# Performance work log

Measured on AMD Instinct MI355X. Metric: run time of the kernel, lower is better.

Reference implementation:

```python
import jax, jax.numpy as jnp
import numpy as np

INIT_RANGE = 0.02

def setup_inputs() -> dict:
    key = jax.random.key(0)
    ks = jax.random.split(key, 5)
    B, S, D, H, Dh = 4, 2048, 768, 12, 64
    residual = jax.random.normal(ks[0], (B, S, D), dtype=jnp.float32)
    W_Q = jax.random.normal(ks[1], (H, D, Dh), dtype=jnp.float32) * INIT_RANGE
    W_K = jax.random.normal(ks[2], (H, D, Dh), dtype=jnp.float32) * INIT_RANGE
    W_V = jax.random.normal(ks[3], (H, D, Dh), dtype=jnp.float32) * INIT_RANGE
    W_O = jax.random.normal(ks[4], (H, Dh, D), dtype=jnp.float32) * INIT_RANGE
    b_Q = jnp.zeros((H, Dh), dtype=jnp.float32)
    b_K = jnp.zeros((H, Dh), dtype=jnp.float32)
    b_V = jnp.zeros((H, Dh), dtype=jnp.float32)
    b_O = jnp.zeros((D,), dtype=jnp.float32)
    return {"residual": residual, "W_Q": W_Q, "W_K": W_K, "W_V": W_V,
            "W_O": W_O, "b_Q": b_Q, "b_K": b_K, "b_V": b_V, "b_O": b_O}

def reference(residual, W_Q, W_K, W_V, W_O, b_Q, b_K, b_V, b_O):
    # residual: [b, s, d]; W_{Q,K,V}: [h, d, dh]; W_O: [h, dh, d]
    d_head = W_Q.shape[-1]
    q = jnp.einsum('bsd,hde->bshe', residual, W_Q) + b_Q  # [b, s, h, dh]
    k = jnp.einsum('bsd,hde->bshe', residual, W_K) + b_K
    v = jnp.einsum('bsd,hde->bshe', residual, W_V) + b_V
    scores = jnp.einsum('bqhe,bkhe->bhqk', q, k) / jnp.sqrt(jnp.float32(d_head))
    S = residual.shape[1]
    causal = jnp.tril(jnp.ones((S, S), dtype=bool))  # True where attending allowed
    scores = jnp.where(causal, scores, -jnp.inf)
    pattern = jax.nn.softmax(scores, axis=-1)  # [b, h, q, k]
    z = jnp.einsum('bkhe,bhqk->bqhe', v, pattern)  # [b, q, h, dh]
    attn_out = jnp.einsum('bqhe,hed->bqd', z, W_O) + b_O
    return attn_out
```

## Files before the change

kernel.cpp:

```cpp
#include <hip/hip_runtime.h>

typedef short short8 __attribute__((ext_vector_type(8)));
typedef float floatx4 __attribute__((ext_vector_type(4)));
typedef unsigned short ushort_t;


__device__ inline ushort_t f2bf(float f) {
  union { float f; unsigned u; } x; x.f = f;
  unsigned u = x.u;
  unsigned r = u + 0x7fffu + ((u >> 16) & 1u);
  return (ushort_t)(r >> 16);
}

__device__ inline unsigned pk2(float a, float b) {
  union { float f; unsigned u; } x, y; x.f = a; y.f = b;
  return ((x.u + 0x8000u) >> 16) | ((y.u + 0x8000u) & 0xffff0000u);
}

__device__ inline float fexp2(float x) {
#if __has_builtin(__builtin_amdgcn_exp2f)
  return __builtin_amdgcn_exp2f(x);
#else
  return exp2f(x);
#endif
}

__device__ inline void async16(const void* g, void* l) {
  __builtin_amdgcn_global_load_lds((const __attribute__((address_space(1))) void*)g,
                                   (__attribute__((address_space(3))) void*)l,
                                   16, 0, 0);
}


__global__ __launch_bounds__(256) void conv_prep(
    const float* __restrict__ x, ushort_t* __restrict__ rx,
    const float* __restrict__ wq, const float* __restrict__ wk, const float* __restrict__ wv,
    const float* __restrict__ wo,
    const float* __restrict__ bq, const float* __restrict__ bk, const float* __restrict__ bv,
    ushort_t* __restrict__ wqkvT, ushort_t* __restrict__ woT, float* __restrict__ bqkv)
{
  __shared__ ushort_t t[64 * 72];
  const int tid = threadIdx.x;
  const int bid0 = blockIdx.x;
  if (bid0 < 6144) {
    int i = bid0 * 256 + tid;
    float4 f = ((const float4*)x)[i];
    ushort4 o;
    o.x = f2bf(f.x); o.y = f2bf(f.y); o.z = f2bf(f.z); o.w = f2bf(f.w);
    ((ushort4*)rx)[i] = o;
    return;
  }
  const int bid = bid0 - 6144;
  if (bid < 432) {
    int m = bid / 144, rem = bid % 144;
    int h = rem / 12, dt = rem % 12;
    int d0 = dt * 64;
    const float* w = (m == 0) ? wq : ((m == 1) ? wk : wv);
    const float* src = w + ((size_t)h * 768 + d0) * 64;
#pragma unroll
    for (int i = 0; i < 4; ++i) {
      int task = i * 256 + tid;
      int row = task >> 4, c4 = task & 15;
      float4 f = *(const float4*)(src + row * 64 + c4 * 4);
      ushort4 o4;
      o4.x = f2bf(f.x); o4.y = f2bf(f.y); o4.z = f2bf(f.z); o4.w = f2bf(f.w);
      *(ushort4*)&t[row * 72 + c4 * 4] = o4;
    }
    __syncthreads();
    ushort_t* dst = wqkvT + ((size_t)m * 768 + h * 64) * 768 + d0;
#pragma unroll
    for (int i = 0; i < 2; ++i) {
      int task = i * 256 + tid;
      int e = task >> 3, sc = task & 7;
      short8 d8;
#pragma unroll
      for (int j = 0; j < 8; ++j) d8[j] = (short)t[(sc * 8 + j) * 72 + e];
      *(short8*)(dst + (size_t)e * 768 + sc * 8) = d8;
    }
  } else if (bid < 576) {
    int b2 = bid - 432;
    int het = b2 / 12, dt = b2 % 12;
    int he0 = het * 64, d0 = dt * 64;
    const float* src = wo + (size_t)he0 * 768 + d0;
#pragma unroll
    for (int i = 0; i < 4; ++i) {
      int task = i * 256 + tid;
      int row = task >> 4, c4 = task & 15;
      float4 f = *(const float4*)(src + (size_t)row * 768 + c4 * 4);
      ushort4 o4;
      o4.x = f2bf(f.x); o4.y = f2bf(f.y); o4.z = f2bf(f.z); o4.w = f2bf(f.w);
      *(ushort4*)&t[row * 72 + c4 * 4] = o4;
    }
    __syncthreads();
    ushort_t* dst = woT + (size_t)d0 * 768 + he0;
#pragma unroll
    for (int i = 0; i < 2; ++i) {
      int task = i * 256 + tid;
      int dd = task >> 3, sc = task & 7;
      short8 d8;
#pragma unroll
      for (int j = 0; j < 8; ++j) d8[j] = (short)t[(sc * 8 + j) * 72 + dd];
      *(short8*)(dst + (size_t)dd * 768 + sc * 8) = d8;
    }
  } else {
    for (int idx = tid; idx < 2304; idx += 256) {
      int m = idx / 768, rem = idx - m * 768;
      const float* bp = (m == 0) ? bq : ((m == 1) ? bk : bv);
      bqkv[idx] = bp[rem];
    }
  }
}


__global__ __launch_bounds__(256) void gemm_qkv(
    const ushort_t* __restrict__ A, const ushort_t* __restrict__ Bt,
    const float* __restrict__ bias,
    ushort_t* __restrict__ q, ushort_t* __restrict__ k, ushort_t* __restrict__ vt)
{
  __shared__ ushort_t sh[17408];
  const int tid = threadIdx.x;
  const int wave = tid >> 6, lane = tid & 63;
  const int ln15 = lane & 15, quad = lane >> 4;
  const int id = blockIdx.x;
  const int xk = id & 7, j = id >> 3;
  const int bx = (xk >> 1) * 16 + (j & 15);
  const int by = (xk & 1) * 9 + (j >> 4);
  const int row0 = bx * 128, col0 = by * 128;
  const int wm = (wave >> 1) * 64, wn = (wave & 1) * 64;
  const int c0 = wave * 2;

  const ushort_t* gA0 = A + (size_t)(row0 + c0 * 16 + (lane >> 2)) * 768 + (lane & 3) * 8;
  const ushort_t* gB0 = Bt + (size_t)(col0 + c0 * 16 + (lane >> 2)) * 768 + (lane & 3) * 8;

  floatx4 acc[4][4];
#pragma unroll
  for (int mi = 0; mi < 4; ++mi)
#pragma unroll
    for (int ni = 0; ni < 4; ++ni)
      acc[mi][ni] = (floatx4){0.f, 0.f, 0.f, 0.f};

  async16(gA0, &sh[c0 * 512]);
  async16(gA0 + 16 * 768, &sh[c0 * 512 + 512]);
  async16(gB0, &sh[8192 + c0 * 512]);
  async16(gB0 + 16 * 768, &sh[8192 + c0 * 512 + 512]);
  __syncthreads();

  for (int kt = 0; kt < 24; ++kt) {
    const int buf = kt & 1;
    if (kt + 1 < 24) {
      ushort_t* dA = &sh[(buf ^ 1) * 4096];
      ushort_t* dB = &sh[8192 + (buf ^ 1) * 4096];
      async16(gA0 + (kt + 1) * 32, dA + c0 * 512);
      async16(gA0 + (kt + 1) * 32 + 16 * 768, dA + c0 * 512 + 512);
      async16(gB0 + (kt + 1) * 32, dB + c0 * 512);
      async16(gB0 + (kt + 1) * 32 + 16 * 768, dB + c0 * 512 + 512);
    }
    const ushort_t* sA = &sh[buf * 4096];
    const ushort_t* sB = &sh[8192 + buf * 4096];
    short8 af[4], bfv[4];
#pragma unroll
    for (int mi = 0; mi < 4; ++mi)
      af[mi] = *(const short8*)&sA[(wm + mi * 16 + ln15) * 32 + quad * 8];
#pragma unroll
    for (int ni = 0; ni < 4; ++ni)
      bfv[ni] = *(const short8*)&sB[(wn + ni * 16 + ln15) * 32 + quad * 8];
#pragma unroll
    for (int mi = 0; mi < 4; ++mi)
#pragma unroll
      for (int ni = 0; ni < 4; ++ni)
        acc[mi][ni] = __builtin_amdgcn_mfma_f32_16x16x32_bf16(af[mi], bfv[ni], acc[mi][ni], 0, 0, 0);
    __syncthreads();
  }

  if (col0 < 1536) {
    const float qscale = 0.125f * 1.44269504f;
#pragma unroll
    for (int mi = 0; mi < 4; ++mi) {
#pragma unroll
      for (int ni = 0; ni < 4; ++ni) {
        int gr = row0 + wm + mi * 16 + quad * 4;
        int gc = col0 + wn + ni * 16 + ln15;
        float bia = bias[gc];
        int m = gc >> 9 >> 1;
        m = gc / 768;
        int rem = gc - m * 768;
        int h = rem >> 6, e = rem & 63;
        ushort_t* dp = (m == 0) ? q : k;
#pragma unroll
        for (int r = 0; r < 4; ++r) {
          float val = acc[mi][ni][r] + bia;
          int rr = gr + r;
          int bb = rr >> 11, ss = rr & 2047;
          size_t dst = ((size_t)((bb * 12 + h) * 2048 + ss) << 6) + e;
          dp[dst] = f2bf((m == 0) ? val * qscale : val);
        }
      }
    }
  } else {
#pragma unroll
    for (int mi = 0; mi < 4; ++mi) {
#pragma unroll
      for (int ni = 0; ni < 4; ++ni) {
        int col = wn + ni * 16 + ln15;
        int rowb = wm + mi * 16 + quad * 4;
        float bia = bias[col0 + col];
        ushort4 w4;
        w4.x = f2bf(acc[mi][ni][0] + bia);
        w4.y = f2bf(acc[mi][ni][1] + bia);
        w4.z = f2bf(acc[mi][ni][2] + bia);
        w4.w = f2bf(acc[mi][ni][3] + bia);
        *(ushort4*)&sh[col * 136 + rowb] = w4;
      }
    }
    __syncthreads();
    const int relc0 = col0 - 1536;
    const int bb = row0 >> 11, s0 = row0 & 2047;
#pragma unroll
    for (int i = 0; i < 8; ++i) {
      int g = i * 256 + tid;
      int col = g >> 4, chunk = g & 15;
      short8 d = *(const short8*)&sh[col * 136 + chunk * 8];
      int hh = (relc0 + col) >> 6;
      int ee = col & 63;
      *(short8*)(vt + (((size_t)(bb * 12 + hh) * 64 + ee) << 11) + s0 + chunk * 8) = d;
    }
  }
}


__global__ __launch_bounds__(256) void gemm_out(
    const ushort_t* __restrict__ A, const ushort_t* __restrict__ Bt,
    const float* __restrict__ bias, float* __restrict__ outf)
{
  __shared__ ushort_t lA[2][64 * 32];
  __shared__ ushort_t lB[2][128 * 32];
  const int tid = threadIdx.x;
  const int wave = tid >> 6, lane = tid & 63;
  const int ln15 = lane & 15, quad = lane >> 4;
  const int id = blockIdx.x;
  const int xk = id & 7, j = id >> 3;
  const int bx = xk * 16 + (j & 15);
  const int by = j >> 4;
  const int row0 = bx * 64, col0 = by * 128;
  const int wm = (wave >> 1) * 32, wn = (wave & 1) * 64;
  const int cb = wave * 2;

  const ushort_t* gA0 = A + (size_t)(row0 + wave * 16 + (lane >> 2)) * 768 + (lane & 3) * 8;
  const ushort_t* gB0 = Bt + (size_t)(col0 + cb * 16 + (lane >> 2)) * 768 + (lane & 3) * 8;

  floatx4 acc[2][4];
#pragma unroll
  for (int mi = 0; mi < 2; ++mi)
#pragma unroll
    for (int ni = 0; ni < 4; ++ni)
      acc[mi][ni] = (floatx4){0.f, 0.f, 0.f, 0.f};

  async16(gA0, &lA[0][wave * 512]);
  async16(gB0, &lB[0][cb * 512]);
  async16(gB0 + 16 * 768, &lB[0][cb * 512 + 512]);
  __syncthreads();

  for (int kt = 0; kt < 24; ++kt) {
    const int buf = kt & 1;
    if (kt + 1 < 24) {
      async16(gA0 + (kt + 1) * 32, &lA[buf ^ 1][wave * 512]);
      async16(gB0 + (kt + 1) * 32, &lB[buf ^ 1][cb * 512]);
      async16(gB0 + (kt + 1) * 32 + 16 * 768, &lB[buf ^ 1][cb * 512 + 512]);
    }
    short8 af[2], bfv[4];
#pragma unroll
    for (int mi = 0; mi < 2; ++mi)
      af[mi] = *(const short8*)&lA[buf][(wm + mi * 16 + ln15) * 32 + quad * 8];
#pragma unroll
    for (int ni = 0; ni < 4; ++ni)
      bfv[ni] = *(const short8*)&lB[buf][(wn + ni * 16 + ln15) * 32 + quad * 8];
#pragma unroll
    for (int mi = 0; mi < 2; ++mi)
#pragma unroll
      for (int ni = 0; ni < 4; ++ni)
        acc[mi][ni] = __builtin_amdgcn_mfma_f32_16x16x32_bf16(af[mi], bfv[ni], acc[mi][ni], 0, 0, 0);
    __syncthreads();
  }

#pragma unroll
  for (int mi = 0; mi < 2; ++mi) {
#pragma unroll
    for (int ni = 0; ni < 4; ++ni) {
      int gr = row0 + wm + mi * 16 + quad * 4;
      int gc = col0 + wn + ni * 16 + ln15;
      float bia = bias[gc];
#pragma unroll
      for (int r = 0; r < 4; ++r)
        outf[(size_t)(gr + r) * 768 + gc] = acc[mi][ni][r] + bia;
    }
  }
}


__device__ inline short8 frag_ld(const ushort_t* t, int row, int ch) {
  return *(const short8*)&t[row * 64 + (((ch ^ row) & 7) * 8)];
}

__global__ __launch_bounds__(256) void attn3(
    const ushort_t* __restrict__ Q, const ushort_t* __restrict__ K,
    const ushort_t* __restrict__ VT, ushort_t* __restrict__ Z)
{
  __shared__ ushort_t lK[2][64 * 64];
  __shared__ ushort_t lV[2][64 * 64];
  __shared__ ushort_t lPQ[128 * 64];
  const int tid = threadIdx.x;
  const int wave = tid >> 6, lane = tid & 63;
  const int ln15 = lane & 15, quad = lane >> 4;
  const int bi = blockIdx.x;
  const int bh = bi % 48;
  const int t = 15 - (bi / 48);
  const int h = bh % 12, b = bh / 12;
  const size_t base = (size_t)bh * 2048 * 64;
  const ushort_t* Qp = Q + base + (size_t)t * 128 * 64;
  const ushort_t* Kp = K + base;
  const ushort_t* Vp = VT + base;
  const int nk = 2 * t + 2;

  const int srow = tid >> 3, slch = tid & 7;
  const int sc_ = slch ^ (srow & 7);

#pragma unroll
  for (int i = 0; i < 4; ++i) {
    int task = i * 256 + tid;
    int row = task >> 3;
    int c = slch ^ (row & 7);
    async16(Qp + row * 64 + c * 8, &lPQ[task * 8]);
  }
  async16(Kp + (size_t)srow * 64 + sc_ * 8, &lK[0][tid * 8]);
  async16(Kp + (size_t)(srow + 32) * 64 + sc_ * 8, &lK[0][(256 + tid) * 8]);
  async16(Vp + (size_t)srow * 2048 + sc_ * 8, &lV[0][tid * 8]);
  async16(Vp + (size_t)(srow + 32) * 2048 + sc_ * 8, &lV[0][(256 + tid) * 8]);

  const ushort_t* kPre0 = Kp + (size_t)(64 + srow) * 64 + sc_ * 8;
  const ushort_t* kPre1 = kPre0 + 32 * 64;
  const ushort_t* vPre0 = Vp + (size_t)srow * 2048 + 64 + sc_ * 8;
  const ushort_t* vPre1 = vPre0 + 32 * 2048;

  __syncthreads();
  short8 qf[2][2];
#pragma unroll
  for (int c = 0; c < 2; ++c) {
    qf[c][0] = frag_ld(lPQ, wave * 32 + c * 16 + ln15, quad);
    qf[c][1] = frag_ld(lPQ, wave * 32 + c * 16 + ln15, quad + 4);
  }
  __syncthreads();

  float l_i[2] = {0.f, 0.f};
  floatx4 o[2][4];
#pragma unroll
  for (int c = 0; c < 2; ++c)
#pragma unroll
    for (int et = 0; et < 4; ++et) o[c][et] = (floatx4){0.f, 0.f, 0.f, 0.f};

  ushort_t* lPw = lPQ + wave * 2048;
  const int qg0 = t * 128 + wave * 32 + ln15;

  for (int kt = 0; kt < nk; ++kt) {
    const int buf = kt & 1;
    if (kt + 1 < nk) {
      ushort_t* dK = lK[buf ^ 1];
      ushort_t* dV = lV[buf ^ 1];
      async16(kPre0, dK + tid * 8);
      async16(kPre1, dK + (256 + tid) * 8);
      async16(vPre0, dV + tid * 8);
      async16(vPre1, dV + (256 + tid) * 8);
      kPre0 += 4096; kPre1 += 4096; vPre0 += 64; vPre1 += 64;
    }

    floatx4 st[2][4];
#pragma unroll
    for (int ni = 0; ni < 4; ++ni) {
      short8 kf0 = frag_ld(lK[buf], ni * 16 + ln15, quad);
      short8 kf1 = frag_ld(lK[buf], ni * 16 + ln15, quad + 4);
#pragma unroll
      for (int c = 0; c < 2; ++c) {
        floatx4 z4 = (floatx4){0.f, 0.f, 0.f, 0.f};
        z4 = __builtin_amdgcn_mfma_f32_16x16x32_bf16(kf0, qf[c][0], z4, 0, 0, 0);
        st[c][ni] = __builtin_amdgcn_mfma_f32_16x16x32_bf16(kf1, qf[c][1], z4, 0, 0, 0);
      }
    }

    const bool masked = (kt >= 2 * t);
#pragma unroll
    for (int c = 0; c < 2; ++c) {
      const int qg = qg0 + c * 16;
      float p[16];
      float rs = 0.f;
#pragma unroll
      for (int ni = 0; ni < 4; ++ni)
#pragma unroll
        for (int r = 0; r < 4; ++r) {
          float x = st[c][ni][r];
          if (masked) {
            int kg = kt * 64 + ni * 16 + quad * 4 + r;
            x = (kg <= qg) ? x : -1e30f;
          }
          float pe = fexp2(x);
          p[ni * 4 + r] = pe;
          rs += pe;
        }
      rs += __shfl_xor(rs, 16);
      rs += __shfl_xor(rs, 32);
      l_i[c] += rs;
      const int rowl = c * 16 + ln15;
#pragma unroll
      for (int ni = 0; ni < 4; ++ni) {
        int chunk = 2 * ni + (quad >> 1);
        int pos = chunk ^ (rowl & 7);
        uint2 w;
        w.x = pk2(p[ni * 4 + 0], p[ni * 4 + 1]);
        w.y = pk2(p[ni * 4 + 2], p[ni * 4 + 3]);
        *(uint2*)&lPw[rowl * 64 + pos * 8 + (quad & 1) * 4] = w;
      }
    }

    short8 pf[2][2];
#pragma unroll
    for (int c = 0; c < 2; ++c) {
      pf[c][0] = frag_ld(lPw, c * 16 + ln15, quad);
      pf[c][1] = frag_ld(lPw, c * 16 + ln15, quad + 4);
    }
#pragma unroll
    for (int et = 0; et < 4; ++et) {
      short8 vf0 = frag_ld(lV[buf], et * 16 + ln15, quad);
      short8 vf1 = frag_ld(lV[buf], et * 16 + ln15, quad + 4);
#pragma unroll
      for (int c = 0; c < 2; ++c) {
        o[c][et] = __builtin_amdgcn_mfma_f32_16x16x32_bf16(vf0, pf[c][0], o[c][et], 0, 0, 0);
        o[c][et] = __builtin_amdgcn_mfma_f32_16x16x32_bf16(vf1, pf[c][1], o[c][et], 0, 0, 0);
      }
    }
    __syncthreads();
  }

#pragma unroll
  for (int c = 0; c < 2; ++c) {
    float inv = 1.f / l_i[c];
    size_t zrow = (size_t)(b * 2048 + t * 128 + wave * 32 + c * 16 + ln15);
#pragma unroll
    for (int et = 0; et < 4; ++et) {
      ushort4 w;
      w.x = f2bf(o[c][et][0] * inv);
      w.y = f2bf(o[c][et][1] * inv);
      w.z = f2bf(o[c][et][2] * inv);
      w.w = f2bf(o[c][et][3] * inv);
      *(ushort4*)&Z[zrow * 768 + h * 64 + et * 16 + quad * 4] = w;
    }
  }
}


extern "C" void kernel_launch(void* const* d_in, const int* in_sizes, int n_in,
                              void* d_out, int out_size, void* d_ws, size_t ws_size,
                              hipStream_t stream)
{
  const float* residual = (const float*)d_in[0];
  const float* W_Q = (const float*)d_in[1];
  const float* W_K = (const float*)d_in[2];
  const float* W_V = (const float*)d_in[3];
  const float* W_O = (const float*)d_in[4];
  const float* b_Q = (const float*)d_in[5];
  const float* b_K = (const float*)d_in[6];
  const float* b_V = (const float*)d_in[7];
  const float* b_O = (const float*)d_in[8];
  float* out = (float*)d_out;

  char* w = (char*)d_ws;
  ushort_t* rx    = (ushort_t*)(w + 0);
  ushort_t* wqkvT = (ushort_t*)(w + 12582912);
  ushort_t* woT   = (ushort_t*)(w + 16121856);
  float*    bqkv  = (float*)   (w + 17301504);
  ushort_t* q     = (ushort_t*)(w + 17310720);
  ushort_t* k     = (ushort_t*)(w + 29893632);
  ushort_t* vt    = (ushort_t*)(w + 55059456);
  ushort_t* z     = rx;

  conv_prep<<<6721, 256, 0, stream>>>(residual, rx, W_Q, W_K, W_V, W_O,
                                      b_Q, b_K, b_V, wqkvT, woT, bqkv);
  gemm_qkv<<<1152, 256, 0, stream>>>(rx, wqkvT, bqkv, q, k, vt);
  attn3<<<768, 256, 0, stream>>>(q, k, vt, z);
  gemm_out<<<768, 256, 0, stream>>>(z, woT, b_O, out);
}
```

Baseline: 221.0 us.

## Keep softmax probabilities in registers by permuting K rows, dropping LDS round-trip

```diff
diff --git a/kernel.cpp b/kernel.cpp
--- a/kernel.cpp
+++ b/kernel.cpp
@@ -12,9 +12,10 @@
   return (ushort_t)(r >> 16);
 }
 
-__device__ inline unsigned pk2(float a, float b) {
-  union { float f; unsigned u; } x, y; x.f = a; y.f = b;
-  return ((x.u + 0x8000u) >> 16) | ((y.u + 0x8000u) & 0xffff0000u);
+__device__ inline unsigned cvtpk(float a, float b) {
+  unsigned r;
+  asm("v_cvt_pk_bf16_f32 %0, %1, %2" : "=v"(r) : "v"(a), "v"(b));
+  return r;
 }
 
 __device__ inline float fexp2(float x) {
@@ -181,8 +182,7 @@
         int gr = row0 + wm + mi * 16 + quad * 4;
         int gc = col0 + wn + ni * 16 + ln15;
         float bia = bias[gc];
-        int m = gc >> 9 >> 1;
-        m = gc / 768;
+        int m = gc / 768;
         int rem = gc - m * 768;
         int h = rem >> 6, e = rem & 63;
         ushort_t* dp = (m == 0) ? q : k;
@@ -307,7 +307,6 @@
 {
   __shared__ ushort_t lK[2][64 * 64];
   __shared__ ushort_t lV[2][64 * 64];
-  __shared__ ushort_t lPQ[128 * 64];
   const int tid = threadIdx.x;
   const int wave = tid >> 6, lane = tid & 63;
   const int ln15 = lane & 15, quad = lane >> 4;
@@ -323,30 +322,35 @@
 
   const int srow = tid >> 3, slch = tid & 7;
   const int sc_ = slch ^ (srow & 7);
+  const int krow = (srow & 3) | ((srow & 0x0C) << 1) | ((srow & 0x10) >> 2);
 
 #pragma unroll
   for (int i = 0; i < 4; ++i) {
     int task = i * 256 + tid;
     int row = task >> 3;
     int c = slch ^ (row & 7);
-    async16(Qp + row * 64 + c * 8, &lPQ[task * 8]);
-  }
-  async16(Kp + (size_t)srow * 64 + sc_ * 8, &lK[0][tid * 8]);
-  async16(Kp + (size_t)(srow + 32) * 64 + sc_ * 8, &lK[0][(256 + tid) * 8]);
+    ushort_t* qdst = (row < 64) ? &lK[1][row * 64 + slch * 8]
+                                : &lV[1][(row - 64) * 64 + slch * 8];
+    async16(Qp + row * 64 + c * 8, qdst);
+  }
+  async16(Kp + (size_t)krow * 64 + sc_ * 8, &lK[0][tid * 8]);
+  async16(Kp + (size_t)(krow + 32) * 64 + sc_ * 8, &lK[0][(256 + tid) * 8]);
   async16(Vp + (size_t)srow * 2048 + sc_ * 8, &lV[0][tid * 8]);
   async16(Vp + (size_t)(srow + 32) * 2048 + sc_ * 8, &lV[0][(256 + tid) * 8]);
 
-  const ushort_t* kPre0 = Kp + (size_t)(64 + srow) * 64 + sc_ * 8;
+  const ushort_t* kPre0 = Kp + (size_t)(64 + krow) * 64 + sc_ * 8;
   const ushort_t* kPre1 = kPre0 + 32 * 64;
   const ushort_t* vPre0 = Vp + (size_t)srow * 2048 + 64 + sc_ * 8;
   const ushort_t* vPre1 = vPre0 + 32 * 2048;
 
   __syncthreads();
+  const ushort_t* qbase = (wave < 2) ? &lK[1][0] : &lV[1][0];
+  const int qrl = (wave & 1) * 32;
   short8 qf[2][2];
 #pragma unroll
   for (int c = 0; c < 2; ++c) {
-    qf[c][0] = frag_ld(lPQ, wave * 32 + c * 16 + ln15, quad);
-    qf[c][1] = frag_ld(lPQ, wave * 32 + c * 16 + ln15, quad + 4);
+    qf[c][0] = frag_ld(qbase, qrl + c * 16 + ln15, quad);
+    qf[c][1] = frag_ld(qbase, qrl + c * 16 + ln15, quad + 4);
   }
   __syncthreads();
 
@@ -357,7 +361,6 @@
 #pragma unroll
     for (int et = 0; et < 4; ++et) o[c][et] = (floatx4){0.f, 0.f, 0.f, 0.f};
 
-  ushort_t* lPw = lPQ + wave * 2048;
   const int qg0 = t * 128 + wave * 32 + ln15;
 
   for (int kt = 0; kt < nk; ++kt) {
@@ -386,45 +389,38 @@
     }
 
     const bool masked = (kt >= 2 * t);
+    short8 pf[2][2];
 #pragma unroll
     for (int c = 0; c < 2; ++c) {
       const int qg = qg0 + c * 16;
       float p[16];
       float rs = 0.f;
 #pragma unroll
-      for (int ni = 0; ni < 4; ++ni)
+      for (int ni = 0; ni < 4; ++ni) {
 #pragma unroll
         for (int r = 0; r < 4; ++r) {
           float x = st[c][ni][r];
           if (masked) {
-            int kg = kt * 64 + ni * 16 + quad * 4 + r;
+            int kg = kt * 64 + (ni >> 1) * 32 + quad * 8 + (ni & 1) * 4 + r;
             x = (kg <= qg) ? x : -1e30f;
           }
-          float pe = fexp2(x);
-          p[ni * 4 + r] = pe;
-          rs += pe;
+          p[ni * 4 + r] = fexp2(x);
         }
+        rs += (p[ni * 4 + 0] + p[ni * 4 + 1]) + (p[ni * 4 + 2] + p[ni * 4 + 3]);
+      }
       rs += __shfl_xor(rs, 16);
       rs += __shfl_xor(rs, 32);
       l_i[c] += rs;
-      const int rowl = c * 16 + ln15;
-#pragma unroll
-      for (int ni = 0; ni < 4; ++ni) {
-        int chunk = 2 * ni + (quad >> 1);
-        int pos = chunk ^ (rowl & 7);
-        uint2 w;
-        w.x = pk2(p[ni * 4 + 0], p[ni * 4 + 1]);
-        w.y = pk2(p[ni * 4 + 2], p[ni * 4 + 3]);
-        *(uint2*)&lPw[rowl * 64 + pos * 8 + (quad & 1) * 4] = w;
-      }
-    }
-
-    short8 pf[2][2];
-#pragma unroll
-    for (int c = 0; c < 2; ++c) {
-      pf[c][0] = frag_ld(lPw, c * 16 + ln15, quad);
-      pf[c][1] = frag_ld(lPw, c * 16 + ln15, quad + 4);
-    }
+      union { unsigned u[4]; short8 s8; } w0, w1;
+#pragma unroll
+      for (int i2 = 0; i2 < 4; ++i2) {
+        w0.u[i2] = cvtpk(p[i2 * 2], p[i2 * 2 + 1]);
+        w1.u[i2] = cvtpk(p[8 + i2 * 2], p[8 + i2 * 2 + 1]);
+      }
+      pf[c][0] = w0.s8;
+      pf[c][1] = w1.s8;
+    }
+
 #pragma unroll
     for (int et = 0; et < 4; ++et) {
       short8 vf0 = frag_ld(lV[buf], et * 16 + ln15, quad);
```

Measured after the change: 210.0 us. -5.0%, faster.
